# Optimization experiments

Measured on AMD Instinct MI355X. Metric: run time of the kernel, lower is better.

The kernel has to match this reference:

```python
import jax, jax.numpy as jnp
import numpy as np

BATCH, SEQ, H, P, HID, CHUNK = 2, 2048, 32, 64, 2048, 256
NORM_EPS = 1e-5


def setup_inputs() -> dict:
    key = jax.random.key(0)
    ks = jax.random.split(key, 10)
    f = lambda k, sh, sc=1.0: jax.random.normal(k, sh, jnp.float32) * sc
    return {
        "hidden_states_ab": f(ks[0], (BATCH, SEQ, HID), 0.02),
        "hidden_states_g": f(ks[1], (BATCH, SEQ, HID), 0.02),
        "q_states": f(ks[2], (BATCH, SEQ, H, P)),
        "k_states": f(ks[3], (BATCH, SEQ, H, P)),
        "v_states": f(ks[4], (BATCH, SEQ, H, P)),
        "dt_w": f(ks[5], (HID, H), 0.02),
        "dt_b": jnp.zeros((H,), jnp.float32),
        "g_w": f(ks[6], (HID, H), 0.02),
        "g_b": jnp.zeros((H,), jnp.float32),
        "A_log": jnp.log(jnp.arange(1, H + 1, dtype=jnp.float32)),
        "dt_bias": jnp.ones((H,), jnp.float32),
        "norm_weight": jnp.ones((H * P,), jnp.float32),
        "o_w": f(ks[7], (H, P, P), 0.02),
        "o_b": jnp.zeros((H, P), jnp.float32),
    }


def _l2norm(x, eps=1e-12):
    # torch F.normalize(p=2, dim=-1): x / max(||x||, eps)
    n = jnp.sqrt(jnp.sum(x * x, axis=-1, keepdims=True))
    return x / jnp.maximum(n, eps)


def _ssd(x, dt, A, Bm, Cm, chunk):
    # x: (b,s,h,p)  dt: (b,s,h) post-softplus  A: (h,)  Bm/Cm: (b,s,h,n)
    b, s, h, p = x.shape
    n = Bm.shape[-1]
    c = s // chunk
    rs = lambda t: t.reshape(b, c, chunk, *t.shape[2:])
    x, dt, Bm, Cm = rs(x), rs(dt), rs(Bm), rs(Cm)
    a = dt * A                         # (b,c,L,h) log-decay increments
    cum = jnp.cumsum(a, axis=2)        # (b,c,L,h)
    cumT = jnp.swapaxes(cum, 2, 3)     # (b,c,h,L)
    # intra-chunk (quadratic, causal) part
    diff = cumT[..., :, None] - cumT[..., None, :]          # (b,c,h,L,L)
    mask = jnp.tril(jnp.ones((chunk, chunk), bool))
    decay = jnp.exp(jnp.where(mask, diff, -jnp.inf))
    CB = jnp.einsum('bclhn,bcshn->bchls', Cm, Bm)
    scores = CB * decay * jnp.swapaxes(dt, 2, 3)[:, :, :, None, :]
    y = jnp.einsum('bchls,bcshp->bclhp', scores, x)
    # per-chunk states
    decay_last = jnp.exp(cumT[..., -1:] - cumT)             # (b,c,h,L)
    w = jnp.swapaxes(decay_last, 2, 3) * dt                 # (b,c,L,h)
    states = jnp.einsum('bclh,bclhn,bclhp->bchpn', w, Bm, x)
    # inter-chunk recurrence over c chunks
    chunk_decay = jnp.exp(cumT[..., -1])                    # (b,c,h)
    def step(Hs, inp):
        cd, st = inp
        return cd[..., None, None] * Hs + st, Hs
    H_last, H_prev = jax.lax.scan(
        step, jnp.zeros((b, h, p, n), x.dtype),
        (jnp.moveaxis(chunk_decay, 1, 0), jnp.moveaxis(states, 1, 0)))
    H_prev = jnp.moveaxis(H_prev, 0, 1)                     # (b,c,h,p,n)
    y = y + jnp.einsum('bclhn,bclh,bchpn->bclhp', Cm, jnp.exp(cum), H_prev)
    return y.reshape(b, s, h, p), H_last


def reference(hidden_states_ab, hidden_states_g, q_states, k_states, v_states,
              dt_w, dt_b, g_w, g_b, A_log, dt_bias, norm_weight, o_w, o_b):
    b, s, h, p = v_states.shape
    Cm = _l2norm(q_states)
    Bm = _l2norm(k_states)
    # dt_proj bias + mamba dt_bias, then softplus (dt_softplus=True)
    dt = jax.nn.softplus(hidden_states_ab @ dt_w + dt_b + dt_bias)   # (b,s,h)
    A = -jnp.exp(A_log)
    y, ssm_state = _ssd(v_states, dt, A, Bm, Cm, CHUNK)
    # gate: g_proj then repeat_interleave(head_dim) on last dim
    gate = jnp.repeat(hidden_states_g @ g_w + g_b, p, axis=-1)       # (b,s,h*p)
    # RMSNormGated, norm_before_gate=False: normalize(x * silu(z)) * weight
    y = y.reshape(b, s, h * p) * jax.nn.silu(gate)
    y = y * jax.lax.rsqrt(jnp.mean(y * y, axis=-1, keepdims=True) + NORM_EPS)
    y = y * norm_weight
    # GroupLinear o_proj: per-head (p -> p) linear
    out = jnp.einsum('bshp,hpq->bshq', y.reshape(b, s, h, p), o_w) + o_b
    return out.reshape(b, s, h * p)
```

## Files before the change

kernel.cpp:

```cpp
#include <hip/hip_runtime.h>
#include <math.h>

#define BATCH 2
#define SEQ   2048
#define NH    32
#define HID   2048
#define CHUNK 256
#define NCH   8
#define NBCH  (BATCH*NCH*NH)
#define PST   72
#define BK    256
#define APST  264
#define KSPLIT 4
#define KSEG  (HID / KSPLIT)

typedef __attribute__((ext_vector_type(4))) float f32x4;
typedef __attribute__((ext_vector_type(8))) short bf16x8;
typedef unsigned int uint;
typedef unsigned short ushort;

__device__ __forceinline__ float softplusf(float x) {
    return x > 20.f ? x : log1pf(expf(x));
}

__device__ __forceinline__ short f2bf(float f) {
    union { float f; uint u; } v; v.f = f;
    uint r = v.u + 0x7FFF + ((v.u >> 16) & 1);
    return (short)(r >> 16);
}
__device__ __forceinline__ float bf2f(ushort s) {
    union { uint u; float f; } v; v.u = ((uint)s) << 16; return v.f;
}
__device__ __forceinline__ uint packbf2(float lo, float hi) {
    uint r;
    asm("v_cvt_pk_bf16_f32 %0, %1, %2" : "=v"(r) : "v"(lo), "v"(hi));
    return r;
}

__device__ __forceinline__ bf16x8 load_cvt8(const float* p, float scale) {
    float4 a = *(const float4*)p;
    float4 b = *(const float4*)(p + 4);
    union { bf16x8 v; uint u[4]; } r;
    r.u[0] = packbf2(a.x * scale, a.y * scale);
    r.u[1] = packbf2(a.z * scale, a.w * scale);
    r.u[2] = packbf2(b.x * scale, b.y * scale);
    r.u[3] = packbf2(b.z * scale, b.w * scale);
    return r.v;
}

__device__ __forceinline__ bf16x8 cvt8(float4 a, float4 b, float s) {
    union { bf16x8 v; uint u[4]; } r;
    r.u[0] = packbf2(a.x * s, a.y * s);
    r.u[1] = packbf2(a.z * s, a.w * s);
    r.u[2] = packbf2(b.x * s, b.y * s);
    r.u[3] = packbf2(b.z * s, b.w * s);
    return r.v;
}

#define MFMA(a,b,c) __builtin_amdgcn_mfma_f32_16x16x32_bf16((a),(b),(c),0,0,0)

__global__ __launch_bounds__(256) void k_proj(
    const float* __restrict__ hs_ab, const float* __restrict__ hs_g,
    const float* __restrict__ dt_w, const float* __restrict__ g_w,
    const float* __restrict__ o_w,  const float* __restrict__ norm_w,
    float* __restrict__ part, short* __restrict__ nwWT)
{
    __shared__ __align__(16) short As[32 * APST];
    __shared__ __align__(16) short Bs[32 * APST];
    int blk = blockIdx.x;
    int t = threadIdx.x;

    if (blk >= 2 * KSPLIT * 128) {
        int h = blk - 2 * KSPLIT * 128;
        float* tile = (float*)As;
        {
            int p = t >> 2, q0 = (t & 3) * 16;
            const float* wp = o_w + (size_t)h * 4096 + p * 64 + q0;
            #pragma unroll
            for (int i = 0; i < 4; ++i)
                *(float4*)(tile + p * 64 + q0 + i * 4) = *(const float4*)(wp + i * 4);
        }
        __syncthreads();
        int q = t >> 2, p0 = (t & 3) * 16;
        uint us[8];
        #pragma unroll
        for (int j = 0; j < 8; ++j) {
            float lo = tile[(p0 + 2*j    ) * 64 + q] * norm_w[h * 64 + p0 + 2*j];
            float hi = tile[(p0 + 2*j + 1) * 64 + q] * norm_w[h * 64 + p0 + 2*j + 1];
            us[j] = packbf2(lo, hi);
        }
        uint* dst = (uint*)(nwWT + (size_t)h * 4096 + q * 64 + p0);
        *(uint4*)dst       = make_uint4(us[0], us[1], us[2], us[3]);
        *(uint4*)(dst + 4) = make_uint4(us[4], us[5], us[6], us[7]);
        return;
    }

    int ksp = blk >> 8;
    int rem = blk & 255;
    int which = rem >> 7;
    int rt = rem & 127;
    int r0 = rt * 32;
    const float* Am = which ? hs_g : hs_ab;
    const float* W  = which ? g_w  : dt_w;
    int w = t >> 6, lane = t & 63, quad = lane >> 4, l16 = lane & 15;
    int mh = w & 1, nh = w >> 1;

    f32x4 acc = (f32x4){0.f, 0.f, 0.f, 0.f};

    for (int kc = ksp * KSEG; kc < ksp * KSEG + KSEG; kc += BK) {
        __syncthreads();
        {
            int row = t >> 3, k0 = (t & 7) * 32;
            const float* src = Am + (size_t)(r0 + row) * HID + kc + k0;
            uint* dst = (uint*)(As + row * APST + k0);
            #pragma unroll
            for (int i = 0; i < 4; ++i) {
                float4 a = *(const float4*)(src + i * 8);
                float4 b = *(const float4*)(src + i * 8 + 4);
                dst[i*4+0] = packbf2(a.x, a.y); dst[i*4+1] = packbf2(a.z, a.w);
                dst[i*4+2] = packbf2(b.x, b.y); dst[i*4+3] = packbf2(b.z, b.w);
            }
        }
        if (t < 128) {
            int k2 = t * 2;
            const float* w0 = W + (size_t)(kc + k2) * NH;
            const float* w1 = w0 + NH;
            #pragma unroll
            for (int n = 0; n < 32; n += 4) {
                float4 a = *(const float4*)(w0 + n);
                float4 b = *(const float4*)(w1 + n);
                *((uint*)(Bs + (n+0) * APST + k2)) = packbf2(a.x, b.x);
                *((uint*)(Bs + (n+1) * APST + k2)) = packbf2(a.y, b.y);
                *((uint*)(Bs + (n+2) * APST + k2)) = packbf2(a.z, b.z);
                *((uint*)(Bs + (n+3) * APST + k2)) = packbf2(a.w, b.w);
            }
        }
        __syncthreads();
        #pragma unroll
        for (int ks = 0; ks < BK / 32; ++ks) {
            bf16x8 af = *(const bf16x8*)(As + (mh*16 + l16) * APST + ks*32 + quad*8);
            bf16x8 bf = *(const bf16x8*)(Bs + (nh*16 + l16) * APST + ks*32 + quad*8);
            acc = MFMA(af, bf, acc);
        }
    }

    int n = nh * 16 + l16;
    int Rb = r0 + mh * 16 + quad * 4;
    float* pd = part + ((size_t)(which * KSPLIT + ksp) * 4096 + Rb) * 32 + n;
    #pragma unroll
    for (int r = 0; r < 4; ++r)
        pd[r * 32] = acc[r];
}

__global__ __launch_bounds__(256) void k_cumsum(
    const float* __restrict__ part, const float* __restrict__ dt_b,
    const float* __restrict__ dt_bias, const float* __restrict__ A_log,
    float* __restrict__ cumc, float* __restrict__ wvc,
    float* __restrict__ dtc, float* __restrict__ cd)
{
    __shared__ float wsum[4];
    int bch = blockIdx.x;
    int h = bch & 31, c = (bch >> 5) & 7, b = bch >> 8;
    int t = threadIdx.x;
    int w = t >> 6, lane = t & 63;
    int rid = (b * SEQ + c * CHUNK + t) * 32 + h;
    float s = part[rid] + part[131072 + rid] + part[262144 + rid] + part[393216 + rid];
    float dt_l = softplusf(s + dt_b[h] + dt_bias[h]);
    float A = -expf(A_log[h]);
    float v = dt_l * A;
    #pragma unroll
    for (int off = 1; off < 64; off <<= 1) {
        float u = __shfl_up(v, off);
        if (lane >= off) v += u;
    }
    if (lane == 63) wsum[w] = v;
    __syncthreads();
    float pre = 0.f;
    #pragma unroll
    for (int i = 0; i < 3; ++i)
        if (i < w) pre += wsum[i];
    float cum = v + pre;
    float tot = wsum[0] + wsum[1] + wsum[2] + wsum[3];
    size_t o = (size_t)bch * CHUNK + t;
    cumc[o] = cum;
    wvc[o] = expf(tot - cum) * dt_l;
    dtc[o] = dt_l;
    if (t == 255) cd[bch] = expf(tot);
}

__global__ __launch_bounds__(256) void k_states(
    const float* __restrict__ kst, const float* __restrict__ vst,
    const float* __restrict__ wvc, float* __restrict__ sp)
{
    __shared__ __align__(16) float kS[64 * 64];
    __shared__ __align__(16) float xS[64 * 64];
    int blk = blockIdx.x;
    int half = blk & 1, bch = blk >> 1;
    int h = bch & 31, c = (bch >> 5) & 7, b = bch >> 8;
    int t = threadIdx.x;
    size_t rowbase = (size_t)b * SEQ + c * CHUNK + half * 128;
    int pg = (t & 15) * 4, ng = (t >> 4) * 4;
    float acc[4][4];
    #pragma unroll
    for (int i = 0; i < 4; ++i)
        #pragma unroll
        for (int j = 0; j < 4; ++j) acc[i][j] = 0.f;

    for (int tt = 0; tt < 2; ++tt) {
        int r0 = t >> 4;
        int c4 = (t & 15) * 4;
        #pragma unroll
        for (int i = 0; i < 4; ++i) {
            int row = r0 + i * 16;
            size_t grow = (rowbase + tt * 64 + row) * NH + h;
            float wv = wvc[(size_t)bch * CHUNK + half * 128 + tt * 64 + row];
            float4 kv = *(const float4*)(kst + grow * 64 + c4);
            float4 xv = *(const float4*)(vst + grow * 64 + c4);
            float ssq = kv.x*kv.x + kv.y*kv.y + kv.z*kv.z + kv.w*kv.w;
            ssq += __shfl_xor(ssq, 1); ssq += __shfl_xor(ssq, 2);
            ssq += __shfl_xor(ssq, 4); ssq += __shfl_xor(ssq, 8);
            float ib = 1.f / fmaxf(sqrtf(ssq), 1e-12f);
            *(float4*)(kS + row * 64 + c4) =
                make_float4(kv.x * ib, kv.y * ib, kv.z * ib, kv.w * ib);
            *(float4*)(xS + row * 64 + c4) =
                make_float4(xv.x * wv, xv.y * wv, xv.z * wv, xv.w * wv);
        }
        __syncthreads();
        for (int ll = 0; ll < 64; ++ll) {
            float4 x4 = *(const float4*)(xS + ll * 64 + pg);
            float4 k4 = *(const float4*)(kS + ll * 64 + ng);
            acc[0][0] += x4.x * k4.x; acc[0][1] += x4.x * k4.y;
            acc[0][2] += x4.x * k4.z; acc[0][3] += x4.x * k4.w;
            acc[1][0] += x4.y * k4.x; acc[1][1] += x4.y * k4.y;
            acc[1][2] += x4.y * k4.z; acc[1][3] += x4.y * k4.w;
            acc[2][0] += x4.z * k4.x; acc[2][1] += x4.z * k4.y;
            acc[2][2] += x4.z * k4.z; acc[2][3] += x4.z * k4.w;
            acc[3][0] += x4.w * k4.x; acc[3][1] += x4.w * k4.y;
            acc[3][2] += x4.w * k4.z; acc[3][3] += x4.w * k4.w;
        }
        __syncthreads();
    }
    size_t obase = (size_t)blk * 4096;
    #pragma unroll
    for (int i = 0; i < 4; ++i)
        *(float4*)(sp + obase + (pg + i) * 64 + ng) =
            make_float4(acc[i][0], acc[i][1], acc[i][2], acc[i][3]);
}

__global__ __launch_bounds__(256) void k_scan(
    const float* __restrict__ sp, const float* __restrict__ cd,
    float* __restrict__ Hp)
{
    size_t id = (size_t)blockIdx.x * 256 + threadIdx.x;
    size_t bh = id >> 12, pn = id & 4095;
    size_t b = bh >> 5, h = bh & 31;
    float carry = 0.f;
    for (int c = 0; c < NCH; ++c) {
        size_t bch = (b * NCH + c) * NH + h;
        float st = sp[(bch * 2) * 4096 + pn] + sp[(bch * 2 + 1) * 4096 + pn];
        Hp[bch * 4096 + pn] = carry;
        carry = cd[bch] * carry + st;
    }
}

__global__ __launch_bounds__(256, 2) void k_intra(
    const float* __restrict__ qst, const float* __restrict__ kst,
    const float* __restrict__ vst,
    const float* __restrict__ cumc, const float* __restrict__ dtc,
    const float* __restrict__ Hp,
    short* __restrict__ ygb)
{
    __shared__ __align__(16) short B_s[2][64 * PST];
    __shared__ __align__(16) short XT_s[2][64 * PST];
    __shared__ __align__(16) short P_s[4 * 32 * PST];
    __shared__ float sCum[256];
    __shared__ float sDt[256];

    int bch = blockIdx.x;
    int h = bch & 31, c = (bch >> 5) & 7, b = bch >> 8;
    int t = threadIdx.x;
    int w = t >> 6, lane = t & 63;
    int quad = lane >> 4, l16 = lane & 15;
    size_t rowbase = (size_t)b * SEQ + c * CHUNK;

    sCum[t] = cumc[(size_t)bch * CHUNK + t];
    sDt[t]  = dtc[(size_t)bch * CHUNK + t];

    int ssA = t >> 2, q4A = (t & 3) * 16;
    int ss2 = t & 31, p0 = (t >> 5) * 8;

    float4 kv[4], xa[2], xb[2];
    {
        size_t gK = (rowbase + ssA) * NH + h;
        const float4* kp = (const float4*)(kst + gK * 64 + q4A);
        kv[0] = kp[0]; kv[1] = kp[1]; kv[2] = kp[2]; kv[3] = kp[3];
        size_t g0 = (rowbase + 2 * ss2) * NH + h;
        const float* vp0 = vst + g0 * 64 + p0;
        const float* vp1 = vst + (g0 + NH) * 64 + p0;
        xa[0] = *(const float4*)vp0; xa[1] = *(const float4*)(vp0 + 4);
        xb[0] = *(const float4*)vp1; xb[1] = *(const float4*)(vp1 + 4);
    }

    bf16x8 cf[2][2][2];
    #pragma unroll
    for (int is = 0; is < 2; ++is) {
        int strip = is ? (7 - w) : w;
        #pragma unroll
        for (int lt = 0; lt < 2; ++lt) {
            int l = strip * 32 + lt * 16 + l16;
            size_t grow = (rowbase + l) * NH + h;
            const float* qp = qst + grow * 64 + quad * 8;
            float4 a  = *(const float4*)qp;
            float4 bq = *(const float4*)(qp + 4);
            float4 c2 = *(const float4*)(qp + 32);
            float4 d  = *(const float4*)(qp + 36);
            float ssq = a.x*a.x + a.y*a.y + a.z*a.z + a.w*a.w
                      + bq.x*bq.x + bq.y*bq.y + bq.z*bq.z + bq.w*bq.w
                      + c2.x*c2.x + c2.y*c2.y + c2.z*c2.z + c2.w*c2.w
                      + d.x*d.x + d.y*d.y + d.z*d.z + d.w*d.w;
            ssq += __shfl_xor(ssq, 16);
            ssq += __shfl_xor(ssq, 32);
            float ic = 1.f / fmaxf(sqrtf(ssq), 1e-12f);
            cf[is][lt][0] = cvt8(a, bq, ic);
            cf[is][lt][1] = cvt8(c2, d, ic);
        }
    }

    f32x4 acc[2][2][4];
    #pragma unroll
    for (int is = 0; is < 2; ++is)
        #pragma unroll
        for (int lt = 0; lt < 2; ++lt)
            #pragma unroll
            for (int pt = 0; pt < 4; ++pt)
                acc[is][lt][pt] = (f32x4){0.f, 0.f, 0.f, 0.f};

    {
        bf16x8 hf[4][2];
        #pragma unroll
        for (int pt = 0; pt < 4; ++pt) {
            const float* hp = Hp + (size_t)bch * 4096 + (pt * 16 + l16) * 64 + quad * 8;
            hf[pt][0] = load_cvt8(hp, 1.f);
            hf[pt][1] = load_cvt8(hp + 32, 1.f);
        }
        #pragma unroll
        for (int is = 0; is < 2; ++is)
            #pragma unroll
            for (int lt = 0; lt < 2; ++lt)
                #pragma unroll
                for (int pt = 0; pt < 4; ++pt) {
                    acc[is][lt][pt] = MFMA(cf[is][lt][0], hf[pt][0], acc[is][lt][pt]);
                    acc[is][lt][pt] = MFMA(cf[is][lt][1], hf[pt][1], acc[is][lt][pt]);
                }
    }
    __syncthreads();
    #pragma unroll
    for (int is = 0; is < 2; ++is) {
        int strip = is ? (7 - w) : w;
        #pragma unroll
        for (int lt = 0; lt < 2; ++lt) {
            float e[4];
            #pragma unroll
            for (int r = 0; r < 4; ++r)
                e[r] = __expf(sCum[strip * 32 + lt * 16 + quad * 4 + r]);
            #pragma unroll
            for (int pt = 0; pt < 4; ++pt)
                #pragma unroll
                for (int r = 0; r < 4; ++r)
                    acc[is][lt][pt][r] *= e[r];
        }
    }

    short* Pw = P_s + w * 32 * PST;

    #pragma unroll
    for (int st = 0; st < 4; ++st) {
        float4 kvN[4], xaN[2], xbN[2];
        if (st < 3) {
            size_t gK = (rowbase + (st + 1) * 64 + ssA) * NH + h;
            const float4* kp = (const float4*)(kst + gK * 64 + q4A);
            kvN[0] = kp[0]; kvN[1] = kp[1]; kvN[2] = kp[2]; kvN[3] = kp[3];
            size_t g0 = (rowbase + (st + 1) * 64 + 2 * ss2) * NH + h;
            const float* vp0 = vst + g0 * 64 + p0;
            const float* vp1 = vst + (g0 + NH) * 64 + p0;
            xaN[0] = *(const float4*)vp0; xaN[1] = *(const float4*)(vp0 + 4);
            xbN[0] = *(const float4*)vp1; xbN[1] = *(const float4*)(vp1 + 4);
        }

        short* Bb = B_s[st & 1];
        short* Xb = XT_s[st & 1];
        {
            float ssq = kv[0].x*kv[0].x + kv[0].y*kv[0].y + kv[0].z*kv[0].z + kv[0].w*kv[0].w
                      + kv[1].x*kv[1].x + kv[1].y*kv[1].y + kv[1].z*kv[1].z + kv[1].w*kv[1].w
                      + kv[2].x*kv[2].x + kv[2].y*kv[2].y + kv[2].z*kv[2].z + kv[2].w*kv[2].w
                      + kv[3].x*kv[3].x + kv[3].y*kv[3].y + kv[3].z*kv[3].z + kv[3].w*kv[3].w;
            ssq += __shfl_xor(ssq, 1);
            ssq += __shfl_xor(ssq, 2);
            float ib = 1.f / fmaxf(sqrtf(ssq), 1e-12f);
            uint u[8];
            u[0] = packbf2(kv[0].x * ib, kv[0].y * ib); u[1] = packbf2(kv[0].z * ib, kv[0].w * ib);
            u[2] = packbf2(kv[1].x * ib, kv[1].y * ib); u[3] = packbf2(kv[1].z * ib, kv[1].w * ib);
            u[4] = packbf2(kv[2].x * ib, kv[2].y * ib); u[5] = packbf2(kv[2].z * ib, kv[2].w * ib);
            u[6] = packbf2(kv[3].x * ib, kv[3].y * ib); u[7] = packbf2(kv[3].z * ib, kv[3].w * ib);
            uint* dst = (uint*)(Bb + ssA * PST + q4A);
            *(uint4*)dst = make_uint4(u[0], u[1], u[2], u[3]);
            *(uint4*)(dst + 4) = make_uint4(u[4], u[5], u[6], u[7]);
        }
        {
            float dt0 = sDt[st * 64 + 2 * ss2];
            float dt1 = sDt[st * 64 + 2 * ss2 + 1];
            float x0[8] = {xa[0].x, xa[0].y, xa[0].z, xa[0].w,
                           xa[1].x, xa[1].y, xa[1].z, xa[1].w};
            float x1[8] = {xb[0].x, xb[0].y, xb[0].z, xb[0].w,
                           xb[1].x, xb[1].y, xb[1].z, xb[1].w};
            uint* xt = (uint*)Xb;
            #pragma unroll
            for (int i = 0; i < 8; ++i)
                xt[(p0 + i) * (PST / 2) + ss2] = packbf2(x0[i] * dt0, x1[i] * dt1);
        }
        __syncthreads();

        bf16x8 xf[4][2];
        #pragma unroll
        for (int pt = 0; pt < 4; ++pt) {
            #pragma unroll
            for (int ks = 0; ks < 2; ++ks)
                xf[pt][ks] = *(const bf16x8*)(Xb + (pt * 16 + l16) * PST + ks * 32 + quad * 8);
        }

        #pragma unroll
        for (int is = 0; is < 2; ++is) {
            int strip = is ? (7 - w) : w;
            int L0 = strip * 32;
            if (L0 + 31 < st * 64) continue;

            #pragma unroll
            for (int lt = 0; lt < 2; ++lt) {
                int Lt = L0 + lt * 16;
                float cl = sCum[Lt + l16];
                int lrow = lt * 16 + l16;
                #pragma unroll
                for (int mt = 0; mt < 4; ++mt) {
                    int S0 = st * 64 + mt * 16;
                    uint* pdst = (uint*)(Pw + lrow * PST + mt * 16 + quad * 4);
                    if (S0 > Lt + 15) {
                        *(uint2*)pdst = make_uint2(0u, 0u);
                        continue;
                    }
                    f32x4 sa = (f32x4){0.f, 0.f, 0.f, 0.f};
                    bf16x8 af0 = *(const bf16x8*)(Bb + (mt * 16 + l16) * PST + quad * 8);
                    bf16x8 af1 = *(const bf16x8*)(Bb + (mt * 16 + l16) * PST + 32 + quad * 8);
                    sa = MFMA(af0, cf[is][lt][0], sa);
                    sa = MFMA(af1, cf[is][lt][1], sa);
                    float vals[4];
                    #pragma unroll
                    for (int r = 0; r < 4; ++r) {
                        int s = S0 + quad * 4 + r;
                        float v = sa[r] * __expf(cl - sCum[s]);
                        vals[r] = (Lt + l16 >= s) ? v : 0.f;
                    }
                    *(uint2*)pdst = make_uint2(packbf2(vals[0], vals[1]),
                                               packbf2(vals[2], vals[3]));
                }
            }
            #pragma unroll
            for (int lt = 0; lt < 2; ++lt) {
                int Lmax = L0 + lt * 16 + 15;
                #pragma unroll
                for (int ks = 0; ks < 2; ++ks) {
                    if (st * 64 + ks * 32 > Lmax) continue;
                    bf16x8 af = *(const bf16x8*)(Pw + (lt * 16 + l16) * PST + ks * 32 + quad * 8);
                    #pragma unroll
                    for (int pt = 0; pt < 4; ++pt)
                        acc[is][lt][pt] = MFMA(af, xf[pt][ks], acc[is][lt][pt]);
                }
            }
        }

        if (st < 3) {
            kv[0] = kvN[0]; kv[1] = kvN[1]; kv[2] = kvN[2]; kv[3] = kvN[3];
            xa[0] = xaN[0]; xa[1] = xaN[1];
            xb[0] = xbN[0]; xb[1] = xbN[1];
        }
    }

    #pragma unroll
    for (int is = 0; is < 2; ++is) {
        int strip = is ? (7 - w) : w;
        #pragma unroll
        for (int lt = 0; lt < 2; ++lt)
            #pragma unroll
            for (int pt = 0; pt < 4; ++pt)
                #pragma unroll
                for (int r = 0; r < 4; ++r) {
                    int l = strip * 32 + lt * 16 + quad * 4 + r;
                    int p = pt * 16 + l16;
                    ygb[((rowbase + l) * NH + h) * 64 + p] = f2bf(acc[is][lt][pt][r]);
                }
    }
}

__global__ __launch_bounds__(256) void k_out(
    const short* __restrict__ ygb, const float* __restrict__ part,
    const float* __restrict__ g_b, const short* __restrict__ nwWT,
    const float* __restrict__ o_b, float* __restrict__ out)
{
    __shared__ __align__(16) short yS[16 * 1024];
    __shared__ float silS[16 * 32];
    __shared__ float scaleS[16];
    int blk = blockIdx.x;
    int half = blk & 1, rt = blk >> 1;
    int r0 = rt * 16;
    int t = threadIdx.x;
    int w = t >> 6, lane = t & 63, quad = lane >> 4, l16 = lane & 15;

    const float* gpart = part + 4 * 131072;
    #pragma unroll
    for (int ii = 0; ii < 2; ++ii) {
        int idx = t + ii * 256;
        int rr = idx >> 5, hh = idx & 31;
        int rid = (r0 + rr) * 32 + hh;
        float g = gpart[rid] + gpart[131072 + rid] + gpart[262144 + rid]
                + gpart[393216 + rid] + g_b[hh];
        silS[idx] = g / (1.f + expf(-g));
    }
    __syncthreads();

    int r = t >> 4, cl = t & 15;
    const char* yrow = (const char*)(ygb + (size_t)(r0 + r) * 2048);
    float ssq = 0.f;
    #pragma unroll
    for (int i = 0; i < 16; ++i) {
        int cb = i * 256 + cl * 16;
        uint4 u = *(const uint4*)(yrow + cb);
        float s = silS[r * 32 + (cb >> 7)];
        float v0 = bf2f((ushort)(u.x & 0xFFFF)) * s, v1 = bf2f((ushort)(u.x >> 16)) * s;
        float v2 = bf2f((ushort)(u.y & 0xFFFF)) * s, v3 = bf2f((ushort)(u.y >> 16)) * s;
        float v4 = bf2f((ushort)(u.z & 0xFFFF)) * s, v5 = bf2f((ushort)(u.z >> 16)) * s;
        float v6 = bf2f((ushort)(u.w & 0xFFFF)) * s, v7 = bf2f((ushort)(u.w >> 16)) * s;
        ssq += v0*v0 + v1*v1 + v2*v2 + v3*v3 + v4*v4 + v5*v5 + v6*v6 + v7*v7;
        if ((cb >> 11) == half) {
            int cbl = cb & 2047;
            *(uint4*)((char*)yS + r * 2048 + (cbl ^ ((r & 7) << 4))) = u;
        }
    }
    ssq += __shfl_xor(ssq, 1); ssq += __shfl_xor(ssq, 2);
    ssq += __shfl_xor(ssq, 4); ssq += __shfl_xor(ssq, 8);
    if (cl == 0) scaleS[r] = rsqrtf(ssq / 2048.f + 1e-5f);
    __syncthreads();

    #pragma unroll
    for (int hh = 0; hh < 4; ++hh) {
        int h = half * 16 + w * 4 + hh;
        int hl = h & 15;
        const short* wb = nwWT + (size_t)h * 4096;
        bf16x8 bfr[4][2];
        #pragma unroll
        for (int nt = 0; nt < 4; ++nt)
            #pragma unroll
            for (int ks = 0; ks < 2; ++ks)
                bfr[nt][ks] = *(const bf16x8*)(wb + (nt * 16 + l16) * 64 + ks * 32 + quad * 8);
        bf16x8 af[2];
        #pragma unroll
        for (int ks = 0; ks < 2; ++ks) {
            int cbl = hl * 128 + ks * 64 + quad * 16;
            af[ks] = *(const bf16x8*)((const char*)yS + l16 * 2048 + (cbl ^ ((l16 & 7) << 4)));
        }
        f32x4 acc[4];
        #pragma unroll
        for (int nt = 0; nt < 4; ++nt) acc[nt] = (f32x4){0.f, 0.f, 0.f, 0.f};
        #pragma unroll
        for (int ks = 0; ks < 2; ++ks)
            #pragma unroll
            for (int nt = 0; nt < 4; ++nt)
                acc[nt] = MFMA(af[ks], bfr[nt][ks], acc[nt]);
        #pragma unroll
        for (int nt = 0; nt < 4; ++nt) {
            float bv = o_b[h * 64 + nt * 16 + l16];
            #pragma unroll
            for (int rr = 0; rr < 4; ++rr) {
                int row = quad * 4 + rr;
                float o = acc[nt][rr] * silS[row * 32 + h] * scaleS[row] + bv;
                out[(size_t)(r0 + row) * 2048 + h * 64 + nt * 16 + l16] = o;
            }
        }
    }
}

extern "C" void kernel_launch(void* const* d_in, const int* in_sizes, int n_in,
                              void* d_out, int out_size, void* d_ws, size_t ws_size,
                              hipStream_t stream) {
    const float* hs_ab   = (const float*)d_in[0];
    const float* hs_g    = (const float*)d_in[1];
    const float* qst     = (const float*)d_in[2];
    const float* kst     = (const float*)d_in[3];
    const float* vst     = (const float*)d_in[4];
    const float* dt_w    = (const float*)d_in[5];
    const float* dt_b    = (const float*)d_in[6];
    const float* g_w     = (const float*)d_in[7];
    const float* g_b     = (const float*)d_in[8];
    const float* A_log   = (const float*)d_in[9];
    const float* dt_bias = (const float*)d_in[10];
    const float* norm_w  = (const float*)d_in[11];
    const float* o_w     = (const float*)d_in[12];
    const float* o_b     = (const float*)d_in[13];
    float* out = (float*)d_out;

    float* ws = (float*)d_ws;
    size_t off = 0;
    float* part   = ws + off; off += (size_t)2 * KSPLIT * 4096 * 32;
    float* cumc   = ws + off; off += (size_t)NBCH * CHUNK;
    float* wvc    = ws + off; off += (size_t)NBCH * CHUNK;
    float* dtc    = ws + off; off += (size_t)NBCH * CHUNK;
    float* cd_ws  = ws + off; off += (size_t)NBCH;
    float* sp     = ws + off; off += (size_t)NBCH * 2 * 4096;
    float* Hp     = ws + off; off += (size_t)NBCH * 4096;
    short* nwWT   = (short*)(ws + off); off += (size_t)NH * 64 * 64 / 2;

    short* ygb = (short*)sp;

    k_proj<<<2 * KSPLIT * (BATCH * SEQ / 32) + NH, 256, 0, stream>>>(
        hs_ab, hs_g, dt_w, g_w, o_w, norm_w, part, nwWT);
    k_cumsum<<<NBCH, 256, 0, stream>>>(part, dt_b, dt_bias, A_log,
                                       cumc, wvc, dtc, cd_ws);
    k_states<<<NBCH * 2, 256, 0, stream>>>(kst, vst, wvc, sp);
    k_scan<<<BATCH * NH * 4096 / 256, 256, 0, stream>>>(sp, cd_ws, Hp);
    k_intra<<<NBCH, 256, 0, stream>>>(qst, kst, vst, cumc, dtc, Hp, ygb);
    k_out<<<2 * (BATCH * SEQ / 16), 256, 0, stream>>>(ygb, part, g_b, nwWT, o_b, out);
}
```

Baseline: 265.2 us.

## Fuse cumsum into state kernel and compute chunk states with bf16 MFMA

Merges the dt/cumsum kernel into the per-chunk state kernel, so each block recomputes the chunk's decay weights locally. This removes one launch and the wvc workspace round-trip. The fp32 scalar outer-product loop is replaced by bf16 MFMA on transposed shared-memory tiles of normalized K and weighted V. Each half-block recomputes the full 256-row scan, which is redundant work, and bf16 rounding of the state inputs lowers precision.

```diff
diff --git a/kernel.cpp b/kernel.cpp
--- a/kernel.cpp
+++ b/kernel.cpp
@@ -152,99 +152,125 @@
         pd[r * 32] = acc[r];
 }
 
-__global__ __launch_bounds__(256) void k_cumsum(
+__global__ __launch_bounds__(256) void k_states(
     const float* __restrict__ part, const float* __restrict__ dt_b,
     const float* __restrict__ dt_bias, const float* __restrict__ A_log,
-    float* __restrict__ cumc, float* __restrict__ wvc,
-    float* __restrict__ dtc, float* __restrict__ cd)
+    const float* __restrict__ kst, const float* __restrict__ vst,
+    float* __restrict__ cumc, float* __restrict__ dtc, float* __restrict__ cd,
+    float* __restrict__ sp)
 {
+    __shared__ __align__(16) short kT[64 * PST];
+    __shared__ __align__(16) short xwT[64 * PST];
     __shared__ float wsum[4];
-    int bch = blockIdx.x;
-    int h = bch & 31, c = (bch >> 5) & 7, b = bch >> 8;
-    int t = threadIdx.x;
-    int w = t >> 6, lane = t & 63;
-    int rid = (b * SEQ + c * CHUNK + t) * 32 + h;
-    float s = part[rid] + part[131072 + rid] + part[262144 + rid] + part[393216 + rid];
-    float dt_l = softplusf(s + dt_b[h] + dt_bias[h]);
-    float A = -expf(A_log[h]);
-    float v = dt_l * A;
-    #pragma unroll
-    for (int off = 1; off < 64; off <<= 1) {
-        float u = __shfl_up(v, off);
-        if (lane >= off) v += u;
-    }
-    if (lane == 63) wsum[w] = v;
-    __syncthreads();
-    float pre = 0.f;
-    #pragma unroll
-    for (int i = 0; i < 3; ++i)
-        if (i < w) pre += wsum[i];
-    float cum = v + pre;
-    float tot = wsum[0] + wsum[1] + wsum[2] + wsum[3];
-    size_t o = (size_t)bch * CHUNK + t;
-    cumc[o] = cum;
-    wvc[o] = expf(tot - cum) * dt_l;
-    dtc[o] = dt_l;
-    if (t == 255) cd[bch] = expf(tot);
-}
-
-__global__ __launch_bounds__(256) void k_states(
-    const float* __restrict__ kst, const float* __restrict__ vst,
-    const float* __restrict__ wvc, float* __restrict__ sp)
-{
-    __shared__ __align__(16) float kS[64 * 64];
-    __shared__ __align__(16) float xS[64 * 64];
+    __shared__ float sWv[256];
+
     int blk = blockIdx.x;
     int half = blk & 1, bch = blk >> 1;
     int h = bch & 31, c = (bch >> 5) & 7, b = bch >> 8;
     int t = threadIdx.x;
-    size_t rowbase = (size_t)b * SEQ + c * CHUNK + half * 128;
-    int pg = (t & 15) * 4, ng = (t >> 4) * 4;
-    float acc[4][4];
-    #pragma unroll
-    for (int i = 0; i < 4; ++i)
-        #pragma unroll
-        for (int j = 0; j < 4; ++j) acc[i][j] = 0.f;
+    int w = t >> 6, lane = t & 63;
+    int quad = lane >> 4, l16 = lane & 15;
+    size_t rowbase = (size_t)b * SEQ + c * CHUNK;
+
+    {
+        int rid = (b * SEQ + c * CHUNK + t) * 32 + h;
+        float s = part[rid] + part[131072 + rid] + part[262144 + rid] + part[393216 + rid];
+        float dt_l = softplusf(s + dt_b[h] + dt_bias[h]);
+        float A = -expf(A_log[h]);
+        float v = dt_l * A;
+        #pragma unroll
+        for (int off = 1; off < 64; off <<= 1) {
+            float u = __shfl_up(v, off);
+            if (lane >= off) v += u;
+        }
+        if (lane == 63) wsum[w] = v;
+        __syncthreads();
+        float pre = 0.f;
+        #pragma unroll
+        for (int i = 0; i < 3; ++i)
+            if (i < w) pre += wsum[i];
+        float cum = v + pre;
+        float tot = wsum[0] + wsum[1] + wsum[2] + wsum[3];
+        sWv[t] = expf(tot - cum) * dt_l;
+        if ((t >> 7) == half) {
+            size_t o = (size_t)bch * CHUNK + t;
+            cumc[o] = cum;
+            dtc[o] = dt_l;
+        }
+        if (half == 1 && t == 255) cd[bch] = expf(tot);
+    }
+    __syncthreads();
+
+    int rowl = t >> 2;
+    int q4 = (t & 3) * 16;
+
+    f32x4 acc[4];
+    #pragma unroll
+    for (int nt = 0; nt < 4; ++nt) acc[nt] = (f32x4){0.f, 0.f, 0.f, 0.f};
 
     for (int tt = 0; tt < 2; ++tt) {
-        int r0 = t >> 4;
-        int c4 = (t & 15) * 4;
-        #pragma unroll
-        for (int i = 0; i < 4; ++i) {
-            int row = r0 + i * 16;
-            size_t grow = (rowbase + tt * 64 + row) * NH + h;
-            float wv = wvc[(size_t)bch * CHUNK + half * 128 + tt * 64 + row];
-            float4 kv = *(const float4*)(kst + grow * 64 + c4);
-            float4 xv = *(const float4*)(vst + grow * 64 + c4);
-            float ssq = kv.x*kv.x + kv.y*kv.y + kv.z*kv.z + kv.w*kv.w;
-            ssq += __shfl_xor(ssq, 1); ssq += __shfl_xor(ssq, 2);
-            ssq += __shfl_xor(ssq, 4); ssq += __shfl_xor(ssq, 8);
+        int r0 = half * 128 + tt * 64;
+        size_t grow = (rowbase + r0 + rowl) * NH + h;
+        {
+            const float4* kp = (const float4*)(kst + grow * 64 + q4);
+            float4 k0 = kp[0], k1 = kp[1], k2 = kp[2], k3 = kp[3];
+            float ssq = k0.x*k0.x + k0.y*k0.y + k0.z*k0.z + k0.w*k0.w
+                      + k1.x*k1.x + k1.y*k1.y + k1.z*k1.z + k1.w*k1.w
+                      + k2.x*k2.x + k2.y*k2.y + k2.z*k2.z + k2.w*k2.w
+                      + k3.x*k3.x + k3.y*k3.y + k3.z*k3.z + k3.w*k3.w;
+            ssq += __shfl_xor(ssq, 1);
+            ssq += __shfl_xor(ssq, 2);
             float ib = 1.f / fmaxf(sqrtf(ssq), 1e-12f);
-            *(float4*)(kS + row * 64 + c4) =
-                make_float4(kv.x * ib, kv.y * ib, kv.z * ib, kv.w * ib);
-            *(float4*)(xS + row * 64 + c4) =
-                make_float4(xv.x * wv, xv.y * wv, xv.z * wv, xv.w * wv);
+            uint u0 = packbf2(k0.x*ib, k0.y*ib), u1 = packbf2(k0.z*ib, k0.w*ib);
+            uint u2 = packbf2(k1.x*ib, k1.y*ib), u3 = packbf2(k1.z*ib, k1.w*ib);
+            uint u4 = packbf2(k2.x*ib, k2.y*ib), u5 = packbf2(k2.z*ib, k2.w*ib);
+            uint u6 = packbf2(k3.x*ib, k3.y*ib), u7 = packbf2(k3.z*ib, k3.w*ib);
+            kT[(q4+ 0)*PST + rowl] = (short)u0; kT[(q4+ 1)*PST + rowl] = (short)(u0>>16);
+            kT[(q4+ 2)*PST + rowl] = (short)u1; kT[(q4+ 3)*PST + rowl] = (short)(u1>>16);
+            kT[(q4+ 4)*PST + rowl] = (short)u2; kT[(q4+ 5)*PST + rowl] = (short)(u2>>16);
+            kT[(q4+ 6)*PST + rowl] = (short)u3; kT[(q4+ 7)*PST + rowl] = (short)(u3>>16);
+            kT[(q4+ 8)*PST + rowl] = (short)u4; kT[(q4+ 9)*PST + rowl] = (short)(u4>>16);
+            kT[(q4+10)*PST + rowl] = (short)u5; kT[(q4+11)*PST + rowl] = (short)(u5>>16);
+            kT[(q4+12)*PST + rowl] = (short)u6; kT[(q4+13)*PST + rowl] = (short)(u6>>16);
+            kT[(q4+14)*PST + rowl] = (short)u7; kT[(q4+15)*PST + rowl] = (short)(u7>>16);
+        }
+        {
+            const float4* xp = (const float4*)(vst + grow * 64 + q4);
+            float4 x0 = xp[0], x1 = xp[1], x2 = xp[2], x3 = xp[3];
+            float wv = sWv[r0 + rowl];
+            uint u0 = packbf2(x0.x*wv, x0.y*wv), u1 = packbf2(x0.z*wv, x0.w*wv);
+            uint u2 = packbf2(x1.x*wv, x1.y*wv), u3 = packbf2(x1.z*wv, x1.w*wv);
+            uint u4 = packbf2(x2.x*wv, x2.y*wv), u5 = packbf2(x2.z*wv, x2.w*wv);
+            uint u6 = packbf2(x3.x*wv, x3.y*wv), u7 = packbf2(x3.z*wv, x3.w*wv);
+            xwT[(q4+ 0)*PST + rowl] = (short)u0; xwT[(q4+ 1)*PST + rowl] = (short)(u0>>16);
+            xwT[(q4+ 2)*PST + rowl] = (short)u1; xwT[(q4+ 3)*PST + rowl] = (short)(u1>>16);
+            xwT[(q4+ 4)*PST + rowl] = (short)u2; xwT[(q4+ 5)*PST + rowl] = (short)(u2>>16);
+            xwT[(q4+ 6)*PST + rowl] = (short)u3; xwT[(q4+ 7)*PST + rowl] = (short)(u3>>16);
+            xwT[(q4+ 8)*PST + rowl] = (short)u4; xwT[(q4+ 9)*PST + rowl] = (short)(u4>>16);
+            xwT[(q4+10)*PST + rowl] = (short)u5; xwT[(q4+11)*PST + rowl] = (short)(u5>>16);
+            xwT[(q4+12)*PST + rowl] = (short)u6; xwT[(q4+13)*PST + rowl] = (short)(u6>>16);
+            xwT[(q4+14)*PST + rowl] = (short)u7; xwT[(q4+15)*PST + rowl] = (short)(u7>>16);
         }
         __syncthreads();
-        for (int ll = 0; ll < 64; ++ll) {
-            float4 x4 = *(const float4*)(xS + ll * 64 + pg);
-            float4 k4 = *(const float4*)(kS + ll * 64 + ng);
-            acc[0][0] += x4.x * k4.x; acc[0][1] += x4.x * k4.y;
-            acc[0][2] += x4.x * k4.z; acc[0][3] += x4.x * k4.w;
-            acc[1][0] += x4.y * k4.x; acc[1][1] += x4.y * k4.y;
-            acc[1][2] += x4.y * k4.z; acc[1][3] += x4.y * k4.w;
-            acc[2][0] += x4.z * k4.x; acc[2][1] += x4.z * k4.y;
-            acc[2][2] += x4.z * k4.z; acc[2][3] += x4.z * k4.w;
-            acc[3][0] += x4.w * k4.x; acc[3][1] += x4.w * k4.y;
-            acc[3][2] += x4.w * k4.z; acc[3][3] += x4.w * k4.w;
+
+        #pragma unroll
+        for (int ks = 0; ks < 2; ++ks) {
+            bf16x8 a = *(const bf16x8*)(xwT + (w*16 + l16)*PST + ks*32 + quad*8);
+            #pragma unroll
+            for (int nt = 0; nt < 4; ++nt) {
+                bf16x8 bb = *(const bf16x8*)(kT + (nt*16 + l16)*PST + ks*32 + quad*8);
+                acc[nt] = MFMA(a, bb, acc[nt]);
+            }
         }
         __syncthreads();
     }
+
     size_t obase = (size_t)blk * 4096;
     #pragma unroll
-    for (int i = 0; i < 4; ++i)
-        *(float4*)(sp + obase + (pg + i) * 64 + ng) =
-            make_float4(acc[i][0], acc[i][1], acc[i][2], acc[i][3]);
+    for (int nt = 0; nt < 4; ++nt)
+        #pragma unroll
+        for (int r = 0; r < 4; ++r)
+            sp[obase + (w*16 + quad*4 + r) * 64 + nt*16 + l16] = acc[nt][r];
 }
 
 __global__ __launch_bounds__(256) void k_scan(
@@ -610,7 +636,6 @@
     size_t off = 0;
     float* part   = ws + off; off += (size_t)2 * KSPLIT * 4096 * 32;
     float* cumc   = ws + off; off += (size_t)NBCH * CHUNK;
-    float* wvc    = ws + off; off += (size_t)NBCH * CHUNK;
     float* dtc    = ws + off; off += (size_t)NBCH * CHUNK;
     float* cd_ws  = ws + off; off += (size_t)NBCH;
     float* sp     = ws + off; off += (size_t)NBCH * 2 * 4096;
@@ -621,9 +646,8 @@
 
     k_proj<<<2 * KSPLIT * (BATCH * SEQ / 32) + NH, 256, 0, stream>>>(
         hs_ab, hs_g, dt_w, g_w, o_w, norm_w, part, nwWT);
-    k_cumsum<<<NBCH, 256, 0, stream>>>(part, dt_b, dt_bias, A_log,
-                                       cumc, wvc, dtc, cd_ws);
-    k_states<<<NBCH * 2, 256, 0, stream>>>(kst, vst, wvc, sp);
+    k_states<<<NBCH * 2, 256, 0, stream>>>(part, dt_b, dt_bias, A_log,
+                                           kst, vst, cumc, dtc, cd_ws, sp);
     k_scan<<<BATCH * NH * 4096 / 256, 256, 0, stream>>>(sp, cd_ws, Hp);
     k_intra<<<NBCH, 256, 0, stream>>>(qst, kst, vst, cumc, dtc, Hp, ygb);
     k_out<<<2 * (BATCH * SEQ / 16), 256, 0, stream>>>(ygb, part, g_b, nwWT, o_b, out);
```

After: 260.5 us. About the same (-1.8%).
